# Kernel optimization log

Measured on AMD Instinct MI355X. Metric: run time of the kernel, lower is better.

Reference implementation:

```python
import jax, jax.numpy as jnp
import numpy as np

B, L, D_MODEL = 2, 1024, 512
N_LAYERS, D_STATE, D_CONV = 6, 16, 4
D_INNER = 2 * D_MODEL          # Mamba default expand=2
DT_RANK = (D_MODEL + 15) // 16  # ceil(d_model/16) = 32
EPS = 1.1920929e-07             # torch RMSNorm default eps (fp32 machine eps)


def rmsnorm(x, w):
    return x * jax.lax.rsqrt(jnp.mean(x * x, axis=-1, keepdims=True) + EPS) * w


def selective_scan(u, dt, A, Bm, Cm, Dv):
    # u, dt: (B,L,E); A: (E,N); Bm, Cm: (B,L,N); Dv: (E,)
    dA = jnp.exp(jnp.einsum('ble,en->blen', dt, A))    # discretized A (ZOH)
    dBu = jnp.einsum('ble,bln->blen', dt * u, Bm)      # discretized B * u (Euler)

    def step(h, inp):
        dA_t, dBu_t, C_t = inp
        h = dA_t * h + dBu_t                           # (B,E,N) state update
        y = jnp.einsum('ben,bn->be', h, C_t)
        return h, y

    h0 = jnp.zeros((u.shape[0], u.shape[2], A.shape[1]), u.dtype)
    _, ys = jax.lax.scan(step, h0,
                         (dA.transpose(1, 0, 2, 3), dBu.transpose(1, 0, 2, 3),
                          Cm.transpose(1, 0, 2)))
    return ys.transpose(1, 0, 2) + u * Dv


def mamba_block(x, p):
    xz = jnp.einsum('bld,ed->ble', x, p['in_proj_w'])  # (B,L,2E)
    xi, z = jnp.split(xz, 2, axis=-1)
    # causal depthwise conv1d (kernel D_CONV) + bias + SiLU
    xc = jnp.pad(xi.transpose(0, 2, 1), ((0, 0), (0, 0), (D_CONV - 1, 0)))
    xc = jax.lax.conv_general_dilated(xc, p['conv_w'][:, None, :], (1,), 'VALID',
                                      feature_group_count=D_INNER)
    xi = jax.nn.silu(xc.transpose(0, 2, 1) + p['conv_b'])
    dbc = jnp.einsum('ble,re->blr', xi, p['x_proj_w'])  # (B,L,R+2N)
    dt, Bm, Cm = jnp.split(dbc, [DT_RANK, DT_RANK + D_STATE], axis=-1)
    dt = jax.nn.softplus(jnp.einsum('blr,er->ble', dt, p['dt_w']) + p['dt_b'])
    y = selective_scan(xi, dt, -jnp.exp(p['A_log']), Bm, Cm, p['D'])
    y = y * jax.nn.silu(z)                              # gate branch
    return jnp.einsum('ble,de->bld', y, p['out_w'])


def setup_inputs() -> dict:
    key = jax.random.key(0)
    ks = jax.random.split(key, 8)
    s = 0.02
    return {
        'x': jax.random.normal(ks[0], (B, L, D_MODEL), jnp.float32),
        'position_embedding': jax.random.normal(ks[1], (B, L, D_MODEL), jnp.float32) * 0.02,
        'norm_w': jnp.ones((D_MODEL,), jnp.float32),
        'in_proj_w': jax.random.normal(ks[2], (N_LAYERS, 2 * D_INNER, D_MODEL), jnp.float32) * s,
        'conv_w': jax.random.normal(ks[3], (N_LAYERS, D_INNER, D_CONV), jnp.float32) * 0.2,
        'conv_b': jnp.zeros((N_LAYERS, D_INNER), jnp.float32),
        'x_proj_w': jax.random.normal(ks[4], (N_LAYERS, DT_RANK + 2 * D_STATE, D_INNER), jnp.float32) * s,
        'dt_w': jax.random.normal(ks[5], (N_LAYERS, D_INNER, DT_RANK), jnp.float32) * s,
        'dt_b': jnp.full((N_LAYERS, D_INNER), -4.6, jnp.float32),  # softplus(dt_b) ~ 0.01
        'A_log': jnp.broadcast_to(
            jnp.log(jnp.arange(1, D_STATE + 1, dtype=jnp.float32)),
            (N_LAYERS, D_INNER, D_STATE)) + jnp.zeros((N_LAYERS, D_INNER, D_STATE), jnp.float32),
        'D': jnp.ones((N_LAYERS, D_INNER), jnp.float32),
        'out_w': jax.random.normal(ks[6], (N_LAYERS, D_MODEL, D_INNER), jnp.float32) * s,
    }


def reference(x, position_embedding, norm_w, in_proj_w, conv_w, conv_b,
              x_proj_w, dt_w, dt_b, A_log, D, out_w):
    stacked = dict(in_proj_w=in_proj_w, conv_w=conv_w, conv_b=conv_b,
                   x_proj_w=x_proj_w, dt_w=dt_w, dt_b=dt_b,
                   A_log=A_log, D=D, out_w=out_w)

    def body(h, p):
        h = h + position_embedding          # added at the start of every layer
        h = mamba_block(rmsnorm(h, norm_w), p)  # NOTE: no residual, per source
        return h, None

    h, _ = jax.lax.scan(body, x, stacked)
    return h
```

## Files before the change

### kernel.cpp

```cpp
#include <hip/hip_runtime.h>
#include <hip/hip_bf16.h>


typedef __attribute__((ext_vector_type(8))) short bf16x8;
typedef __attribute__((ext_vector_type(4))) float f32x4;

__device__ __forceinline__ float bf2f(unsigned short u) {
    unsigned int x = ((unsigned int)u) << 16;
    return __builtin_bit_cast(float, x);
}
__device__ __forceinline__ unsigned short f2bf(float f) {
    __hip_bfloat16 h = __float2bfloat16(f);
    return __builtin_bit_cast(unsigned short, h);
}
__device__ __forceinline__ float ldin(const void* p, size_t i, int isbf) {
    return isbf ? bf2f(((const unsigned short*)p)[i]) : ((const float*)p)[i];
}
__device__ __forceinline__ float softplus_f(float x) {
    return (x > 20.f) ? x : log1pf(__expf(x));
}
__device__ __forceinline__ void split2(float x, unsigned short& h, unsigned short& l) {
    h = f2bf(x);
    l = f2bf(x - bf2f(h));
}

#define S1 (6*2048*512)
#define S2 (6*512*1024)
#define S3 (6*64*1024)
__global__ __launch_bounds__(256) void wsplit_all(
    const void* __restrict__ ipw, const void* __restrict__ ow,
    const void* __restrict__ xpw, const void* __restrict__ Dw,
    unsigned short* __restrict__ h1, unsigned short* __restrict__ l1,
    unsigned short* __restrict__ h2, unsigned short* __restrict__ l2,
    unsigned short* __restrict__ h3, unsigned short* __restrict__ l3,
    int* __restrict__ flag)
{
    int g = blockIdx.x * 256 + threadIdx.x;
    const int isbf = (*(const unsigned int*)Dw == 0x3F800000u) ? 0 : 1;
    if (g == 0) *flag = isbf;
    const void* src; unsigned short *dh, *dl; int i;
    if (g < S1)             { src = ipw; dh = h1; dl = l1; i = g; }
    else if (g < S1+S2)     { src = ow;  dh = h2; dl = l2; i = g - S1; }
    else if (g < S1+S2+S3)  { src = xpw; dh = h3; dl = l3; i = g - S1 - S2; }
    else return;
    unsigned short hh, ll;
    split2(ldin(src, i, isbf), hh, ll);
    dh[i] = hh; dl[i] = ll;
}

__global__ __launch_bounds__(256) void gemm_in(
    const unsigned short* __restrict__ Ah, const unsigned short* __restrict__ Al,
    const unsigned short* __restrict__ Wh, const unsigned short* __restrict__ Wl,
    long woff,
    float* __restrict__ xf, unsigned short* __restrict__ zg)
{
    __shared__ __align__(16) unsigned short As[2][128][40];
    __shared__ __align__(16) unsigned short Ws[2][64][40];

    const int m0 = blockIdx.x * 128, n0 = blockIdx.y * 64;
    const int t = threadIdx.x, lane = t & 63, wave = t >> 6;
    const int wm = (wave & 1) * 64, wn = (wave >> 1) * 32;
    const int sra = t >> 1, sca = (t & 1) * 16;
    const int srw = t >> 2, scw = (t & 3) * 8;

    const unsigned short* ah = Ah + (size_t)(m0 + sra) * 512 + sca;
    const unsigned short* al = Al + (size_t)(m0 + sra) * 512 + sca;
    const unsigned short* wh = Wh + woff + (size_t)(n0 + srw) * 512 + scw;
    const unsigned short* wl = Wl + woff + (size_t)(n0 + srw) * 512 + scw;

    f32x4 acc[4][2] = {};
    const int fm = lane & 15, fk = (lane >> 4) * 8;

    for (int k0 = 0; k0 < 512; k0 += 32) {
        __syncthreads();
        *(uint4*)(&As[0][sra][sca])     = *(const uint4*)(ah + k0);
        *(uint4*)(&As[0][sra][sca + 8]) = *(const uint4*)(ah + k0 + 8);
        *(uint4*)(&As[1][sra][sca])     = *(const uint4*)(al + k0);
        *(uint4*)(&As[1][sra][sca + 8]) = *(const uint4*)(al + k0 + 8);
        *(uint4*)(&Ws[0][srw][scw])     = *(const uint4*)(wh + k0);
        *(uint4*)(&Ws[1][srw][scw])     = *(const uint4*)(wl + k0);
        __syncthreads();

        bf16x8 a_h[4], a_l[4], w_h[2], w_l[2];
#pragma unroll
        for (int i = 0; i < 4; ++i) {
            a_h[i] = *(const bf16x8*)(&As[0][wm + i * 16 + fm][fk]);
            a_l[i] = *(const bf16x8*)(&As[1][wm + i * 16 + fm][fk]);
        }
#pragma unroll
        for (int i = 0; i < 2; ++i) {
            w_h[i] = *(const bf16x8*)(&Ws[0][wn + i * 16 + fm][fk]);
            w_l[i] = *(const bf16x8*)(&Ws[1][wn + i * 16 + fm][fk]);
        }
#pragma unroll
        for (int mi = 0; mi < 4; ++mi)
#pragma unroll
            for (int ni = 0; ni < 2; ++ni) {
                acc[mi][ni] = __builtin_amdgcn_mfma_f32_16x16x32_bf16(
                    a_h[mi], w_h[ni], acc[mi][ni], 0, 0, 0);
                acc[mi][ni] = __builtin_amdgcn_mfma_f32_16x16x32_bf16(
                    a_h[mi], w_l[ni], acc[mi][ni], 0, 0, 0);
                acc[mi][ni] = __builtin_amdgcn_mfma_f32_16x16x32_bf16(
                    a_l[mi], w_h[ni], acc[mi][ni], 0, 0, 0);
            }
    }

    const int col = lane & 15, rb = (lane >> 4) * 4;
    const int zhalf = (n0 >= 1024);
#pragma unroll
    for (int mi = 0; mi < 4; ++mi)
#pragma unroll
        for (int ni = 0; ni < 2; ++ni)
#pragma unroll
            for (int r = 0; r < 4; ++r) {
                int gm = m0 + wm + mi * 16 + rb + r;
                int gn = n0 + wn + ni * 16 + col;
                float v = acc[mi][ni][r];
                if (!zhalf) {
                    xf[(size_t)gm * 1024 + gn] = v;
                } else {
                    float sv = v / (1.f + __expf(-v));
                    zg[(size_t)gm * 1024 + (gn - 1024)] = f2bf(sv);
                }
            }
}

__global__ __launch_bounds__(256) void gemm_hl(
    const unsigned short* __restrict__ Ah, const unsigned short* __restrict__ Al,
    int lda,
    const unsigned short* __restrict__ Wh, const unsigned short* __restrict__ Wl,
    long woff,
    float* __restrict__ Cf, long zstride,
    int N, int K, int Kc)
{
    __shared__ __align__(16) unsigned short As[2][64][40];
    __shared__ __align__(16) unsigned short Ws[2][64][40];

    const int m0 = blockIdx.x * 64, n0 = blockIdx.y * 64;
    const int kb = blockIdx.z * Kc;
    const int t = threadIdx.x;
    const int lane = t & 63, wave = t >> 6;
    const int wm = (wave & 1) * 32, wn = (wave >> 1) * 32;
    const int srow = t >> 2, scol = (t & 3) * 8;

    const unsigned short* ah = Ah + (size_t)(m0 + srow) * lda + scol;
    const unsigned short* al = Al + (size_t)(m0 + srow) * lda + scol;
    const unsigned short* wh = Wh + woff + (size_t)(n0 + srow) * K + scol;
    const unsigned short* wl = Wl + woff + (size_t)(n0 + srow) * K + scol;

    f32x4 acc[2][2] = {};

    for (int k0 = kb; k0 < kb + Kc; k0 += 32) {
        __syncthreads();
        *(uint4*)(&As[0][srow][scol]) = *(const uint4*)(ah + k0);
        *(uint4*)(&As[1][srow][scol]) = *(const uint4*)(al + k0);
        *(uint4*)(&Ws[0][srow][scol]) = *(const uint4*)(wh + k0);
        *(uint4*)(&Ws[1][srow][scol]) = *(const uint4*)(wl + k0);
        __syncthreads();

        const int fm = lane & 15, fk = (lane >> 4) * 8;
        bf16x8 a0h = *(const bf16x8*)(&As[0][wm + fm][fk]);
        bf16x8 a1h = *(const bf16x8*)(&As[0][wm + 16 + fm][fk]);
        bf16x8 w0h = *(const bf16x8*)(&Ws[0][wn + fm][fk]);
        bf16x8 w1h = *(const bf16x8*)(&Ws[0][wn + 16 + fm][fk]);
        bf16x8 a0l = *(const bf16x8*)(&As[1][wm + fm][fk]);
        bf16x8 a1l = *(const bf16x8*)(&As[1][wm + 16 + fm][fk]);
        bf16x8 w0l = *(const bf16x8*)(&Ws[1][wn + fm][fk]);
        bf16x8 w1l = *(const bf16x8*)(&Ws[1][wn + 16 + fm][fk]);

        acc[0][0] = __builtin_amdgcn_mfma_f32_16x16x32_bf16(a0h, w0h, acc[0][0], 0, 0, 0);
        acc[0][1] = __builtin_amdgcn_mfma_f32_16x16x32_bf16(a0h, w1h, acc[0][1], 0, 0, 0);
        acc[1][0] = __builtin_amdgcn_mfma_f32_16x16x32_bf16(a1h, w0h, acc[1][0], 0, 0, 0);
        acc[1][1] = __builtin_amdgcn_mfma_f32_16x16x32_bf16(a1h, w1h, acc[1][1], 0, 0, 0);
        acc[0][0] = __builtin_amdgcn_mfma_f32_16x16x32_bf16(a0h, w0l, acc[0][0], 0, 0, 0);
        acc[0][1] = __builtin_amdgcn_mfma_f32_16x16x32_bf16(a0h, w1l, acc[0][1], 0, 0, 0);
        acc[1][0] = __builtin_amdgcn_mfma_f32_16x16x32_bf16(a1h, w0l, acc[1][0], 0, 0, 0);
        acc[1][1] = __builtin_amdgcn_mfma_f32_16x16x32_bf16(a1h, w1l, acc[1][1], 0, 0, 0);
        acc[0][0] = __builtin_amdgcn_mfma_f32_16x16x32_bf16(a0l, w0h, acc[0][0], 0, 0, 0);
        acc[0][1] = __builtin_amdgcn_mfma_f32_16x16x32_bf16(a0l, w1h, acc[0][1], 0, 0, 0);
        acc[1][0] = __builtin_amdgcn_mfma_f32_16x16x32_bf16(a1l, w0h, acc[1][0], 0, 0, 0);
        acc[1][1] = __builtin_amdgcn_mfma_f32_16x16x32_bf16(a1l, w1h, acc[1][1], 0, 0, 0);
    }

    float* Cp = Cf + (size_t)blockIdx.z * zstride;
    const int col = lane & 15, rb = (lane >> 4) * 4;
#pragma unroll
    for (int mi = 0; mi < 2; ++mi)
#pragma unroll
        for (int ni = 0; ni < 2; ++ni)
#pragma unroll
            for (int r = 0; r < 4; ++r) {
                int gm = m0 + wm + mi * 16 + rb + r;
                int gn = n0 + wn + ni * 16 + col;
                Cp[(size_t)gm * N + gn] = acc[mi][ni][r];
            }
}

__global__ __launch_bounds__(256) void xp_reduce(
    const float* __restrict__ Pxp, float* __restrict__ dbc)
{
    int g = blockIdx.x * 256 + threadIdx.x;
    float s = 0.f;
#pragma unroll
    for (int z = 0; z < 8; ++z) s += Pxp[(size_t)z * 131072 + g];
    dbc[g] = s;
}

__global__ __launch_bounds__(256) void dt_k(
    const float* __restrict__ dbc,
    const void* __restrict__ dtw, long dtwoff,
    const void* __restrict__ dtb, long dtboff,
    const int* __restrict__ flag,
    float* __restrict__ dtf)
{
    const int isbf = *flag;
    __shared__ float lds[256][33];
    const int tid = threadIdx.x;
    const int e0 = blockIdx.x * 256;
    const int t0 = blockIdx.y * 16;

    for (int idx = tid; idx < 256 * 32; idx += 256)
        lds[idx >> 5][idx & 31] = ldin(dtw, dtwoff + (size_t)e0 * 32 + idx, isbf);
    __syncthreads();

    float wr[32];
#pragma unroll
    for (int r = 0; r < 32; ++r) wr[r] = lds[tid][r];
    float bias = ldin(dtb, dtboff + e0 + tid, isbf);

#pragma unroll
    for (int j = 0; j < 16; ++j) {
        int t = t0 + j;
        const float4* Rp = (const float4*)(dbc + (size_t)t * 64);
        float s = bias;
#pragma unroll
        for (int q = 0; q < 8; ++q) {
            float4 rq = Rp[q];
            s += rq.x * wr[q*4] + rq.y * wr[q*4+1] + rq.z * wr[q*4+2] + rq.w * wr[q*4+3];
        }
        dtf[(size_t)t * 1024 + e0 + tid] = softplus_f(s);
    }
}

__global__ __launch_bounds__(256) void rmsnorm_k(
    const void* __restrict__ hsrc, int hdyn, const void* __restrict__ pos,
    const void* __restrict__ nw, const int* __restrict__ flag,
    unsigned short* __restrict__ xnh, unsigned short* __restrict__ xnl)
{
    const int isbf = *flag;
    const int row = blockIdx.x;
    const int t = threadIdx.x;
    const size_t base = (size_t)row * 512;
    float h0 = hdyn ? ldin(hsrc, base + t, isbf)       : ((const float*)hsrc)[base + t];
    float h1 = hdyn ? ldin(hsrc, base + 256 + t, isbf) : ((const float*)hsrc)[base + 256 + t];
    float v0 = h0 + ldin(pos, base + t, isbf);
    float v1 = h1 + ldin(pos, base + 256 + t, isbf);
    float ss = v0 * v0 + v1 * v1;
#pragma unroll
    for (int o = 32; o; o >>= 1) ss += __shfl_xor(ss, o, 64);
    __shared__ float sw[4];
    if ((t & 63) == 0) sw[t >> 6] = ss;
    __syncthreads();
    float tot = sw[0] + sw[1] + sw[2] + sw[3];
    float sc = rsqrtf(tot * (1.0f / 512.0f) + 1.1920929e-07f);
    float o0 = v0 * sc * ldin(nw, t, isbf);
    float o1 = v1 * sc * ldin(nw, 256 + t, isbf);
    unsigned short hh, ll;
    split2(o0, hh, ll); xnh[base + t] = hh;       xnl[base + t] = ll;
    split2(o1, hh, ll); xnh[base + 256 + t] = hh; xnl[base + 256 + t] = ll;
}

__global__ __launch_bounds__(256) void conv_silu_k(
    const float* __restrict__ xf,
    const void* __restrict__ cw, long cwoff,
    const void* __restrict__ cb, long cboff,
    const int* __restrict__ flag,
    unsigned short* __restrict__ xih, unsigned short* __restrict__ xil)
{
    const int isbf = *flag;
    int g = blockIdx.x * 256 + threadIdx.x;
    int e = g & 1023;
    int l = (g >> 10) & 1023;
    int b = g >> 20;
    float acc = ldin(cb, cboff + e, isbf);
#pragma unroll
    for (int k = 0; k < 4; ++k) {
        int ls = l - 3 + k;
        if (ls >= 0)
            acc += ldin(cw, cwoff + e * 4 + k, isbf) *
                   xf[((size_t)(b * 1024 + ls)) * 1024 + e];
    }
    acc = acc / (1.f + __expf(-acc));
    unsigned short hh, ll;
    split2(acc, hh, ll);
    xih[g] = hh; xil[g] = ll;
}

#define CL 16
#define NCH 64

__global__ __launch_bounds__(256) void scan_stage1(
    const float* __restrict__ dtp,
    const unsigned short* __restrict__ xih, const unsigned short* __restrict__ xil,
    const float* __restrict__ dbc,
    const void* __restrict__ alog, long aoff, const int* __restrict__ flag,
    float* __restrict__ P, float* __restrict__ S)
{
    const int isbf = *flag;
    int g = blockIdx.x * 256 + threadIdx.x;
    int e = g & 1023, c = (g >> 10) & (NCH - 1), b = g >> 16;
    int t0 = b * 1024 + c * CL;

    float dv[CL], uv[CL];
#pragma unroll
    for (int i = 0; i < CL; ++i) {
        size_t ix = (size_t)(t0 + i) * 1024 + e;
        dv[i] = dtp[ix];
        uv[i] = bf2f(xih[ix]) + bf2f(xil[ix]);
    }

    float Aen[16], Pn[16], Sn[16];
#pragma unroll
    for (int n = 0; n < 16; ++n) {
        Aen[n] = -__expf(ldin(alog, aoff + e * 16 + n, isbf));
        Pn[n] = 1.f; Sn[n] = 0.f;
    }
#pragma unroll
    for (int i = 0; i < CL; ++i) {
        float d = dv[i], du = d * uv[i];
        const float4* Bp = (const float4*)(dbc + (size_t)(t0 + i) * 64 + 32);
        float4 b0 = Bp[0], b1 = Bp[1], b2 = Bp[2], b3 = Bp[3];
        float Bt[16] = {b0.x,b0.y,b0.z,b0.w, b1.x,b1.y,b1.z,b1.w,
                        b2.x,b2.y,b2.z,b2.w, b3.x,b3.y,b3.z,b3.w};
#pragma unroll
        for (int n = 0; n < 16; ++n) {
            float a = __expf(d * Aen[n]);
            Sn[n] = a * Sn[n] + du * Bt[n];
            Pn[n] *= a;
        }
    }
    size_t ob = ((size_t)(b * NCH + c) * 16) * 1024 + e;
#pragma unroll
    for (int n = 0; n < 16; ++n) {
        P[ob + (size_t)n * 1024] = Pn[n];
        S[ob + (size_t)n * 1024] = Sn[n];
    }
}

__global__ __launch_bounds__(256) void scan_stage2(
    float* __restrict__ PH, const float* __restrict__ S)
{
    int g = blockIdx.x * 256 + threadIdx.x;
    int e = g & 1023, n = (g >> 10) & 15, b = g >> 14;
    float H = 0.f;
    for (int cb = 0; cb < NCH; cb += 8) {
        float p[8], s[8];
#pragma unroll
        for (int j = 0; j < 8; ++j) {
            size_t idx = ((size_t)(b * NCH + cb + j) * 16 + n) * 1024 + e;
            p[j] = PH[idx]; s[j] = S[idx];
        }
#pragma unroll
        for (int j = 0; j < 8; ++j) {
            size_t idx = ((size_t)(b * NCH + cb + j) * 16 + n) * 1024 + e;
            PH[idx] = H;
            H = p[j] * H + s[j];
        }
    }
}

__global__ __launch_bounds__(256) void scan_stage3(
    const float* __restrict__ dtp,
    const unsigned short* __restrict__ xih, const unsigned short* __restrict__ xil,
    const float* __restrict__ dbc,
    const void* __restrict__ alog, long aoff,
    const void* __restrict__ Dv, long doff,
    const int* __restrict__ flag,
    const unsigned short* __restrict__ zg, const float* __restrict__ H0,
    unsigned short* __restrict__ yh, unsigned short* __restrict__ yl)
{
    const int isbf = *flag;
    int g = blockIdx.x * 256 + threadIdx.x;
    int e = g & 1023, c = (g >> 10) & (NCH - 1), b = g >> 16;
    int t0 = b * 1024 + c * CL;

    float dv[CL], uv[CL], gv[CL];
#pragma unroll
    for (int i = 0; i < CL; ++i) {
        size_t ix = (size_t)(t0 + i) * 1024 + e;
        dv[i] = dtp[ix];
        uv[i] = bf2f(xih[ix]) + bf2f(xil[ix]);
        gv[i] = bf2f(zg[ix]);
    }

    float Aen[16], h[16];
    size_t ob = ((size_t)(b * NCH + c) * 16) * 1024 + e;
#pragma unroll
    for (int n = 0; n < 16; ++n) {
        Aen[n] = -__expf(ldin(alog, aoff + e * 16 + n, isbf));
        h[n] = H0[ob + (size_t)n * 1024];
    }
    float De = ldin(Dv, doff + e, isbf);
#pragma unroll
    for (int i = 0; i < CL; ++i) {
        float d = dv[i], uu = uv[i], du = d * uu;
        const float4* Bp = (const float4*)(dbc + (size_t)(t0 + i) * 64 + 32);
        float4 b0 = Bp[0], b1 = Bp[1], b2 = Bp[2], b3 = Bp[3];
        float4 c0 = Bp[4], c1 = Bp[5], c2 = Bp[6], c3 = Bp[7];
        float Bt[16] = {b0.x,b0.y,b0.z,b0.w, b1.x,b1.y,b1.z,b1.w,
                        b2.x,b2.y,b2.z,b2.w, b3.x,b3.y,b3.z,b3.w};
        float Ct[16] = {c0.x,c0.y,c0.z,c0.w, c1.x,c1.y,c1.z,c1.w,
                        c2.x,c2.y,c2.z,c2.w, c3.x,c3.y,c3.z,c3.w};
        float y = 0.f;
#pragma unroll
        for (int n = 0; n < 16; ++n) {
            float a = __expf(d * Aen[n]);
            h[n] = a * h[n] + du * Bt[n];
            y += h[n] * Ct[n];
        }
        float yv = (y + uu * De) * gv[i];
        unsigned short hh, ll;
        split2(yv, hh, ll);
        yh[(size_t)(t0 + i) * 1024 + e] = hh;
        yl[(size_t)(t0 + i) * 1024 + e] = ll;
    }
}

extern "C" void kernel_launch(void* const* d_in, const int* in_sizes, int n_in,
                              void* d_out, int out_size, void* d_ws, size_t ws_size,
                              hipStream_t stream)
{
    const void* x    = d_in[0];
    const void* pos  = d_in[1];
    const void* nw   = d_in[2];
    const void* ipw  = d_in[3];
    const void* cw   = d_in[4];
    const void* cb   = d_in[5];
    const void* xpw  = d_in[6];
    const void* dtw  = d_in[7];
    const void* dtb  = d_in[8];
    const void* alog = d_in[9];
    const void* Dw   = d_in[10];
    const void* ow   = d_in[11];

    char* w = (char*)d_ws;
    auto take = [&](size_t bytes) { char* p = w; w += (bytes + 255) & ~255ull; return p; };

    float* h    = (float*)take(2048ull * 512 * 4);
    float* xf   = (float*)take(2048ull * 1024 * 4);
    unsigned short* zg = (unsigned short*)take(2048ull * 1024 * 2);
    float* dbc  = (float*)take(2048ull * 64 * 4);
    float* dtf  = (float*)take(2048ull * 1024 * 4);
    float* P    = (float*)take(2ull * NCH * 16 * 1024 * 4);
    float* S    = (float*)take(2ull * NCH * 16 * 1024 * 4);
    float* Pxp  = (float*)take(8ull * 2048 * 64 * 4);
    unsigned short* xnh = (unsigned short*)take(2048ull * 512 * 2);
    unsigned short* xnl = (unsigned short*)take(2048ull * 512 * 2);
    unsigned short* xih = (unsigned short*)take(2048ull * 1024 * 2);
    unsigned short* xil = (unsigned short*)take(2048ull * 1024 * 2);
    unsigned short* yh  = (unsigned short*)take(2048ull * 1024 * 2);
    unsigned short* yl  = (unsigned short*)take(2048ull * 1024 * 2);
    unsigned short* wip_h = (unsigned short*)take(6ull * 2048 * 512 * 2);
    unsigned short* wip_l = (unsigned short*)take(6ull * 2048 * 512 * 2);
    unsigned short* wow_h = (unsigned short*)take(6ull * 512 * 1024 * 2);
    unsigned short* wow_l = (unsigned short*)take(6ull * 512 * 1024 * 2);
    unsigned short* wxp_h = (unsigned short*)take(6ull * 64 * 1024 * 2);
    unsigned short* wxp_l = (unsigned short*)take(6ull * 64 * 1024 * 2);
    int* flag = (int*)take(256);

    wsplit_all<<<(S1 + S2 + S3 + 255) / 256, 256, 0, stream>>>(
        ipw, ow, xpw, Dw,
        wip_h, wip_l, wow_h, wow_l, wxp_h, wxp_l, flag);

    for (int l = 0; l < 6; ++l) {
        rmsnorm_k<<<2048, 256, 0, stream>>>(
            l == 0 ? x : (const void*)h, l == 0 ? 1 : 0, pos, nw, flag, xnh, xnl);
        gemm_in<<<dim3(16, 32), 256, 0, stream>>>(
            xnh, xnl, wip_h, wip_l, (long)l * 2048 * 512, xf, zg);
        conv_silu_k<<<8192, 256, 0, stream>>>(xf, cw, (long)l * 4096, cb, (long)l * 1024,
                                              flag, xih, xil);
        gemm_hl<<<dim3(32, 1, 8), 256, 0, stream>>>(
            xih, xil, 1024, wxp_h, wxp_l, (long)l * 64 * 1024,
            Pxp, 2048l * 64, 64, 1024, 128);
        xp_reduce<<<512, 256, 0, stream>>>(Pxp, dbc);
        dt_k<<<dim3(4, 128), 256, 0, stream>>>(dbc, dtw, (long)l * 1024 * 32,
                                               dtb, (long)l * 1024, flag, dtf);
        scan_stage1<<<512, 256, 0, stream>>>(
            dtf, xih, xil, dbc, alog, (long)l * 16384, flag, P, S);
        scan_stage2<<<128, 256, 0, stream>>>(P, S);
        scan_stage3<<<512, 256, 0, stream>>>(
            dtf, xih, xil, dbc, alog, (long)l * 16384,
            Dw, (long)l * 1024, flag, zg, P, yh, yl);
        float* outp = (l < 5) ? h : (float*)d_out;
        gemm_hl<<<dim3(32, 8), 256, 0, stream>>>(
            yh, yl, 1024, wow_h, wow_l, (long)l * 512 * 1024,
            outp, 0, 512, 1024, 1024);
    }
}
```

Baseline: 936.0 us.

## Fuse split-K reduction into dt kernel and split scan state across two threads

The x_proj split-K partial reduction is folded into the dt projection kernel, which sums the eight partials into shared memory and has one block column write dbc, removing a launch. The scan stage1 and stage3 kernels now split the 16 state dimensions across two threads per channel, doubling the thread count and halving per-thread registers and serial work. Stage3 combines the two halves through shared memory before applying the D skip, gate and output split. In exchange, reloads of dt/u are duplicated across halves, half the threads idle during the epilogue, and there is an added barrier.

```diff
diff --git a/kernel.cpp b/kernel.cpp
--- a/kernel.cpp
+++ b/kernel.cpp
@@ -196,49 +196,51 @@
             }
 }
 
-__global__ __launch_bounds__(256) void xp_reduce(
-    const float* __restrict__ Pxp, float* __restrict__ dbc)
-{
-    int g = blockIdx.x * 256 + threadIdx.x;
-    float s = 0.f;
-#pragma unroll
-    for (int z = 0; z < 8; ++z) s += Pxp[(size_t)z * 131072 + g];
-    dbc[g] = s;
-}
-
-__global__ __launch_bounds__(256) void dt_k(
-    const float* __restrict__ dbc,
+__global__ __launch_bounds__(256) void dtred_k(
+    const float* __restrict__ Pxp, float* __restrict__ dbc,
     const void* __restrict__ dtw, long dtwoff,
     const void* __restrict__ dtb, long dtboff,
     const int* __restrict__ flag,
     float* __restrict__ dtf)
 {
     const int isbf = *flag;
-    __shared__ float lds[256][33];
+    __shared__ float ldbc[16][68];
+    __shared__ float ldsw[256][33];
     const int tid = threadIdx.x;
     const int e0 = blockIdx.x * 256;
     const int t0 = blockIdx.y * 16;
 
+    {
+        int tt = tid >> 4, nn = tid & 15;
+        float sx = 0.f, sy = 0.f, sz = 0.f, sw = 0.f;
+#pragma unroll
+        for (int z = 0; z < 8; ++z) {
+            const float4 v = *(const float4*)(Pxp + (size_t)z * 131072
+                                              + (size_t)(t0 + tt) * 64 + nn * 4);
+            sx += v.x; sy += v.y; sz += v.z; sw += v.w;
+        }
+        ldbc[tt][nn * 4 + 0] = sx; ldbc[tt][nn * 4 + 1] = sy;
+        ldbc[tt][nn * 4 + 2] = sz; ldbc[tt][nn * 4 + 3] = sw;
+        if (blockIdx.x == 0) {
+            float4 o; o.x = sx; o.y = sy; o.z = sz; o.w = sw;
+            *(float4*)(dbc + (size_t)(t0 + tt) * 64 + nn * 4) = o;
+        }
+    }
     for (int idx = tid; idx < 256 * 32; idx += 256)
-        lds[idx >> 5][idx & 31] = ldin(dtw, dtwoff + (size_t)e0 * 32 + idx, isbf);
+        ldsw[idx >> 5][idx & 31] = ldin(dtw, dtwoff + (size_t)e0 * 32 + idx, isbf);
     __syncthreads();
 
     float wr[32];
 #pragma unroll
-    for (int r = 0; r < 32; ++r) wr[r] = lds[tid][r];
+    for (int r = 0; r < 32; ++r) wr[r] = ldsw[tid][r];
     float bias = ldin(dtb, dtboff + e0 + tid, isbf);
 
 #pragma unroll
     for (int j = 0; j < 16; ++j) {
-        int t = t0 + j;
-        const float4* Rp = (const float4*)(dbc + (size_t)t * 64);
         float s = bias;
 #pragma unroll
-        for (int q = 0; q < 8; ++q) {
-            float4 rq = Rp[q];
-            s += rq.x * wr[q*4] + rq.y * wr[q*4+1] + rq.z * wr[q*4+2] + rq.w * wr[q*4+3];
-        }
-        dtf[(size_t)t * 1024 + e0 + tid] = softplus_f(s);
+        for (int q = 0; q < 32; ++q) s += ldbc[j][q] * wr[q];
+        dtf[(size_t)(t0 + j) * 1024 + e0 + tid] = softplus_f(s);
     }
 }
 
@@ -307,8 +309,11 @@
     float* __restrict__ P, float* __restrict__ S)
 {
     const int isbf = *flag;
-    int g = blockIdx.x * 256 + threadIdx.x;
-    int e = g & 1023, c = (g >> 10) & (NCH - 1), b = g >> 16;
+    int bid = blockIdx.x;
+    int eb = bid & 7, c = (bid >> 3) & 63, b = bid >> 9;
+    int tid = threadIdx.x;
+    int e = eb * 128 + (tid & 127);
+    int nb = (tid >> 7) * 8;
     int t0 = b * 1024 + c * CL;
 
     float dv[CL], uv[CL];
@@ -319,29 +324,28 @@
         uv[i] = bf2f(xih[ix]) + bf2f(xil[ix]);
     }
 
-    float Aen[16], Pn[16], Sn[16];
-#pragma unroll
-    for (int n = 0; n < 16; ++n) {
-        Aen[n] = -__expf(ldin(alog, aoff + e * 16 + n, isbf));
+    float Aen[8], Pn[8], Sn[8];
+#pragma unroll
+    for (int n = 0; n < 8; ++n) {
+        Aen[n] = -__expf(ldin(alog, aoff + e * 16 + nb + n, isbf));
         Pn[n] = 1.f; Sn[n] = 0.f;
     }
 #pragma unroll
     for (int i = 0; i < CL; ++i) {
         float d = dv[i], du = d * uv[i];
-        const float4* Bp = (const float4*)(dbc + (size_t)(t0 + i) * 64 + 32);
-        float4 b0 = Bp[0], b1 = Bp[1], b2 = Bp[2], b3 = Bp[3];
-        float Bt[16] = {b0.x,b0.y,b0.z,b0.w, b1.x,b1.y,b1.z,b1.w,
-                        b2.x,b2.y,b2.z,b2.w, b3.x,b3.y,b3.z,b3.w};
-#pragma unroll
-        for (int n = 0; n < 16; ++n) {
+        const float4* Bp = (const float4*)(dbc + (size_t)(t0 + i) * 64 + 32 + nb);
+        float4 b0 = Bp[0], b1 = Bp[1];
+        float Bt[8] = {b0.x, b0.y, b0.z, b0.w, b1.x, b1.y, b1.z, b1.w};
+#pragma unroll
+        for (int n = 0; n < 8; ++n) {
             float a = __expf(d * Aen[n]);
             Sn[n] = a * Sn[n] + du * Bt[n];
             Pn[n] *= a;
         }
     }
-    size_t ob = ((size_t)(b * NCH + c) * 16) * 1024 + e;
-#pragma unroll
-    for (int n = 0; n < 16; ++n) {
+    size_t ob = ((size_t)(b * NCH + c) * 16 + nb) * 1024 + e;
+#pragma unroll
+    for (int n = 0; n < 8; ++n) {
         P[ob + (size_t)n * 1024] = Pn[n];
         S[ob + (size_t)n * 1024] = Sn[n];
     }
@@ -380,49 +384,68 @@
     unsigned short* __restrict__ yh, unsigned short* __restrict__ yl)
 {
     const int isbf = *flag;
-    int g = blockIdx.x * 256 + threadIdx.x;
-    int e = g & 1023, c = (g >> 10) & (NCH - 1), b = g >> 16;
+    __shared__ float ybuf[128][17];
+    int bid = blockIdx.x;
+    int eb = bid & 7, c = (bid >> 3) & 63, b = bid >> 9;
+    int tid = threadIdx.x;
+    int el = tid & 127;
+    int e = eb * 128 + el;
+    int half = tid >> 7;
+    int nb = half * 8;
     int t0 = b * 1024 + c * CL;
 
-    float dv[CL], uv[CL], gv[CL];
+    float dv[CL], uv[CL];
 #pragma unroll
     for (int i = 0; i < CL; ++i) {
         size_t ix = (size_t)(t0 + i) * 1024 + e;
         dv[i] = dtp[ix];
         uv[i] = bf2f(xih[ix]) + bf2f(xil[ix]);
-        gv[i] = bf2f(zg[ix]);
-    }
-
-    float Aen[16], h[16];
-    size_t ob = ((size_t)(b * NCH + c) * 16) * 1024 + e;
-#pragma unroll
-    for (int n = 0; n < 16; ++n) {
-        Aen[n] = -__expf(ldin(alog, aoff + e * 16 + n, isbf));
+    }
+
+    float Aen[8], h[8];
+    size_t ob = ((size_t)(b * NCH + c) * 16 + nb) * 1024 + e;
+#pragma unroll
+    for (int n = 0; n < 8; ++n) {
+        Aen[n] = -__expf(ldin(alog, aoff + e * 16 + nb + n, isbf));
         h[n] = H0[ob + (size_t)n * 1024];
     }
-    float De = ldin(Dv, doff + e, isbf);
+
+    float yv[CL];
 #pragma unroll
     for (int i = 0; i < CL; ++i) {
-        float d = dv[i], uu = uv[i], du = d * uu;
-        const float4* Bp = (const float4*)(dbc + (size_t)(t0 + i) * 64 + 32);
-        float4 b0 = Bp[0], b1 = Bp[1], b2 = Bp[2], b3 = Bp[3];
-        float4 c0 = Bp[4], c1 = Bp[5], c2 = Bp[6], c3 = Bp[7];
-        float Bt[16] = {b0.x,b0.y,b0.z,b0.w, b1.x,b1.y,b1.z,b1.w,
-                        b2.x,b2.y,b2.z,b2.w, b3.x,b3.y,b3.z,b3.w};
-        float Ct[16] = {c0.x,c0.y,c0.z,c0.w, c1.x,c1.y,c1.z,c1.w,
-                        c2.x,c2.y,c2.z,c2.w, c3.x,c3.y,c3.z,c3.w};
+        float d = dv[i], du = d * uv[i];
+        const float4* Bp = (const float4*)(dbc + (size_t)(t0 + i) * 64 + 32 + nb);
+        const float4* Cp = (const float4*)(dbc + (size_t)(t0 + i) * 64 + 48 + nb);
+        float4 b0 = Bp[0], b1 = Bp[1];
+        float4 c0 = Cp[0], c1 = Cp[1];
+        float Bt[8] = {b0.x, b0.y, b0.z, b0.w, b1.x, b1.y, b1.z, b1.w};
+        float Ct[8] = {c0.x, c0.y, c0.z, c0.w, c1.x, c1.y, c1.z, c1.w};
         float y = 0.f;
 #pragma unroll
-        for (int n = 0; n < 16; ++n) {
+        for (int n = 0; n < 8; ++n) {
             float a = __expf(d * Aen[n]);
             h[n] = a * h[n] + du * Bt[n];
             y += h[n] * Ct[n];
         }
-        float yv = (y + uu * De) * gv[i];
-        unsigned short hh, ll;
-        split2(yv, hh, ll);
-        yh[(size_t)(t0 + i) * 1024 + e] = hh;
-        yl[(size_t)(t0 + i) * 1024 + e] = ll;
+        yv[i] = y;
+    }
+
+    if (half == 1) {
+#pragma unroll
+        for (int i = 0; i < CL; ++i) ybuf[el][i] = yv[i];
+    }
+    __syncthreads();
+    if (half == 0) {
+        float De = ldin(Dv, doff + e, isbf);
+#pragma unroll
+        for (int i = 0; i < CL; ++i) {
+            size_t ix = (size_t)(t0 + i) * 1024 + e;
+            float yt = (yv[i] + ybuf[el][i] + uv[i] * De) * bf2f(zg[ix]);
+            unsigned short hh, ll;
+            split2(yt, hh, ll);
+            yh[ix] = hh;
+            yl[ix] = ll;
+        }
     }
 }
 
@@ -482,13 +505,12 @@
         gemm_hl<<<dim3(32, 1, 8), 256, 0, stream>>>(
             xih, xil, 1024, wxp_h, wxp_l, (long)l * 64 * 1024,
             Pxp, 2048l * 64, 64, 1024, 128);
-        xp_reduce<<<512, 256, 0, stream>>>(Pxp, dbc);
-        dt_k<<<dim3(4, 128), 256, 0, stream>>>(dbc, dtw, (long)l * 1024 * 32,
-                                               dtb, (long)l * 1024, flag, dtf);
-        scan_stage1<<<512, 256, 0, stream>>>(
+        dtred_k<<<dim3(4, 128), 256, 0, stream>>>(
+            Pxp, dbc, dtw, (long)l * 1024 * 32, dtb, (long)l * 1024, flag, dtf);
+        scan_stage1<<<1024, 256, 0, stream>>>(
             dtf, xih, xil, dbc, alog, (long)l * 16384, flag, P, S);
         scan_stage2<<<128, 256, 0, stream>>>(P, S);
-        scan_stage3<<<512, 256, 0, stream>>>(
+        scan_stage3<<<1024, 256, 0, stream>>>(
             dtf, xih, xil, dbc, alog, (long)l * 16384,
             Dw, (long)l * 1024, flag, zg, P, yh, yl);
         float* outp = (l < 5) ? h : (float*)d_out;
```

New measurement: 916.9 us. 1.02x faster.
